# Optimization experiments

Hardware: AMD Instinct MI355X
Metric: run time of the kernel (lower is better)

Reference implementation:

```python
import jax, jax.numpy as jnp
import numpy as np

B, S, D = 4, 2048, 512
H = 8
DH = D // H
NEG = -9e15


def setup_inputs() -> dict:
    key = jax.random.key(0)
    ks = jax.random.split(key, 6)
    x = jax.random.normal(ks[0], (B, S, D), dtype=jnp.float32)
    mask = jax.random.randint(ks[1], (B, S), 0, 2, dtype=jnp.int32)
    # Linear params (torch convention: W [out, in], y = x @ W.T + b)
    lim_qkv = 1.0 / np.sqrt(D)
    W_qkv = jax.random.uniform(ks[2], (3 * D, D), jnp.float32, -lim_qkv, lim_qkv)
    b_qkv = jax.random.uniform(ks[3], (3 * D,), jnp.float32, -lim_qkv, lim_qkv)
    lim_o = 1.0 / np.sqrt(D)
    W_o = jax.random.uniform(ks[4], (D, D), jnp.float32, -lim_o, lim_o)
    b_o = jax.random.uniform(ks[5], (D,), jnp.float32, -lim_o, lim_o)
    return {"x": x, "mask": mask, "W_qkv": W_qkv, "b_qkv": b_qkv, "W_o": W_o, "b_o": b_o}


def reference(x, mask, W_qkv, b_qkv, W_o, b_o):
    b, s, d = x.shape
    # fused QKV projection: [B,S,3D]
    qkv = jnp.einsum('bsd,ed->bse', x, W_qkv) + b_qkv
    qkv = qkv.reshape(b, s, H, 3 * DH).transpose(0, 2, 1, 3)  # [B,H,S,3*DH]
    q, k, v = jnp.split(qkv, 3, axis=-1)  # each [B,H,S,DH]
    logits = jnp.einsum('bhqd,bhkd->bhqk', q, k) / jnp.sqrt(jnp.float32(DH))
    m = mask[:, None, None, :]  # [B,1,1,S]
    logits = jnp.where(m == 0, jnp.float32(NEG), logits)
    attn = jax.nn.softmax(logits, axis=-1)  # [B,H,S,S]
    values = jnp.einsum('bhqk,bhkd->bhqd', attn, v)
    values = values.transpose(0, 2, 1, 3).reshape(b, s, d)
    o = jnp.einsum('bsd,ed->bse', values, W_o) + b_o
    return o
```

## Files before the change

### kernel.cpp

```cpp
#include <hip/hip_runtime.h>
#include <stdint.h>

#define Bv 4
#define Sv 2048
#define Dv 512
#define Hv 8
#define E3 1536

typedef unsigned short u16;
typedef __bf16 bf16x8 __attribute__((ext_vector_type(8)));
typedef float f32x4 __attribute__((ext_vector_type(4)));

__device__ __forceinline__ u16 f2b(float f) {
  union { float f; uint32_t u; } v; v.f = f;
  uint32_t r = v.u + 0x7FFFu + ((v.u >> 16) & 1u);
  return (u16)(r >> 16);
}

__device__ __forceinline__ void gl_lds16(const void* g, void* l) {
  __builtin_amdgcn_global_load_lds(
      (__attribute__((address_space(1))) void*)(uintptr_t)g,
      (__attribute__((address_space(3))) void*)(uintptr_t)l, 16, 0, 0);
}

__global__ __launch_bounds__(256) void k_cast3(const float* __restrict__ x,
                                               const float* __restrict__ wqkv,
                                               const float* __restrict__ wo,
                                               const int* __restrict__ mask,
                                               u16* __restrict__ xb,
                                               u16* __restrict__ wqkvb,
                                               u16* __restrict__ wob,
                                               float* __restrict__ mbias) {
  const int bid = blockIdx.x;
  if (bid >= 2560) {
    const int i = (bid - 2560) * 256 + threadIdx.x;
    mbias[i] = mask[i] ? 0.0f : -1e30f;
    return;
  }
  const float* in; u16* out; int i;
  if (bid < 2048)      { in = x;    out = xb;    i = bid * 256 + threadIdx.x; }
  else if (bid < 2432) { in = wqkv; out = wqkvb; i = (bid - 2048) * 256 + threadIdx.x; }
  else                 { in = wo;   out = wob;   i = (bid - 2432) * 256 + threadIdx.x; }
  const float4* p = (const float4*)in;
  float4 a = p[(size_t)i * 2], b = p[(size_t)i * 2 + 1];
  union { u16 h[8]; uint4 v; } r;
  r.h[0] = f2b(a.x); r.h[1] = f2b(a.y); r.h[2] = f2b(a.z); r.h[3] = f2b(a.w);
  r.h[4] = f2b(b.x); r.h[5] = f2b(b.y); r.h[6] = f2b(b.z); r.h[7] = f2b(b.w);
  ((uint4*)out)[i] = r.v;
}

__global__ __launch_bounds__(256) void k_gemm_qkv(const u16* __restrict__ A,
                                                  const u16* __restrict__ Bw,
                                                  const float* __restrict__ bias,
                                                  u16* __restrict__ qp,
                                                  u16* __restrict__ kp,
                                                  u16* __restrict__ vp) {
  const int K = Dv, N = E3;
  __shared__ alignas(16) u16 As[128][32];
  __shared__ alignas(16) u16 Bs[128][32];
  const int tid = threadIdx.x, lane = tid & 63, w = tid >> 6;
  const int quad = lane >> 4, l16 = lane & 15;
  const int wm = w & 1, wn = w >> 1;
  const size_t m0 = (size_t)blockIdx.y * 128;
  const int n0 = blockIdx.x * 128;
  const int srow = lane >> 2, scol = (lane & 3) * 8;
  f32x4 acc[4][4] = {};
  for (int k0 = 0; k0 < K; k0 += 32) {
    #pragma unroll
    for (int c = 0; c < 2; ++c) {
      const int rb = (w * 2 + c) * 16;
      gl_lds16(A + (m0 + rb + srow) * K + k0 + scol, &As[rb][0]);
      gl_lds16(Bw + (size_t)(n0 + rb + srow) * K + k0 + scol, &Bs[rb][0]);
    }
    __syncthreads();
    bf16x8 af[4], bfr[4];
    #pragma unroll
    for (int t = 0; t < 4; ++t) {
      af[t]  = *(const bf16x8*)&As[wm * 64 + t * 16 + l16][quad * 8];
      bfr[t] = *(const bf16x8*)&Bs[wn * 64 + t * 16 + l16][quad * 8];
    }
    #pragma unroll
    for (int mt = 0; mt < 4; ++mt)
      #pragma unroll
      for (int nt = 0; nt < 4; ++nt)
        acc[mt][nt] = __builtin_amdgcn_mfma_f32_16x16x32_bf16(af[mt], bfr[nt],
                                                              acc[mt][nt], 0, 0, 0);
    __syncthreads();
  }
  #pragma unroll
  for (int nt = 0; nt < 4; ++nt) {
    const int cbase = n0 + wn * 64 + nt * 16;
    const int h = cbase / 192, rem = cbase % 192;
    const int region = rem >> 6;
    const int dh = (rem & 63) + l16;
    const float bv = bias[cbase + l16];
    #pragma unroll
    for (int mt = 0; mt < 4; ++mt) {
      #pragma unroll
      for (int r = 0; r < 4; ++r) {
        const int row = (int)m0 + wm * 64 + mt * 16 + quad * 4 + r;
        const u16 vb = f2b(acc[mt][nt][r] + bv);
        const int b = row >> 11, s = row & 2047;
        const size_t bhb = ((size_t)(b * 8 + h)) * 131072;
        if (region == 0) {
          qp[(size_t)row * 512 + h * 64 + dh] = vb;
        } else if (region == 1) {
          kp[bhb + (s >> 4) * 1024 + (dh >> 5) * 512 + ((dh >> 3) & 3) * 128 +
             (s & 15) * 8 + (dh & 7)] = vb;
        } else {
          vp[bhb + (s >> 5) * 2048 + (dh >> 4) * 512 + ((s >> 3) & 3) * 128 +
             (dh & 15) * 8 + (s & 7)] = vb;
        }
      }
    }
  }
}

__global__ __launch_bounds__(256) void k_gemm_out(const u16* __restrict__ A,
                                                  const u16* __restrict__ Bw,
                                                  const float* __restrict__ bias,
                                                  float* __restrict__ C) {
  const int K = Dv, N = Dv;
  __shared__ alignas(16) u16 As[64][32];
  __shared__ alignas(16) u16 Bs[128][32];
  const int tid = threadIdx.x, lane = tid & 63, w = tid >> 6;
  const int quad = lane >> 4, l16 = lane & 15;
  const size_t m0 = (size_t)blockIdx.y * 64;
  const int n0 = blockIdx.x * 128;
  const int srow = lane >> 2, scol = (lane & 3) * 8;
  f32x4 acc[4][2] = {};
  for (int k0 = 0; k0 < K; k0 += 32) {
    gl_lds16(A + (m0 + w * 16 + srow) * K + k0 + scol, &As[w * 16][0]);
    #pragma unroll
    for (int c = 0; c < 2; ++c) {
      const int rb = w * 32 + c * 16;
      gl_lds16(Bw + (size_t)(n0 + rb + srow) * K + k0 + scol, &Bs[rb][0]);
    }
    __syncthreads();
    bf16x8 af[4], bfr[2];
    #pragma unroll
    for (int t = 0; t < 4; ++t) af[t] = *(const bf16x8*)&As[t * 16 + l16][quad * 8];
    #pragma unroll
    for (int t = 0; t < 2; ++t)
      bfr[t] = *(const bf16x8*)&Bs[w * 32 + t * 16 + l16][quad * 8];
    #pragma unroll
    for (int mt = 0; mt < 4; ++mt)
      #pragma unroll
      for (int nt = 0; nt < 2; ++nt)
        acc[mt][nt] = __builtin_amdgcn_mfma_f32_16x16x32_bf16(af[mt], bfr[nt],
                                                              acc[mt][nt], 0, 0, 0);
    __syncthreads();
  }
  #pragma unroll
  for (int nt = 0; nt < 2; ++nt) {
    const int col = n0 + w * 32 + nt * 16 + l16;
    const float bv = bias[col];
    #pragma unroll
    for (int mt = 0; mt < 4; ++mt) {
      const size_t row = m0 + mt * 16 + quad * 4;
      #pragma unroll
      for (int r = 0; r < 4; ++r) C[(row + r) * N + col] = acc[mt][nt][r] + bv;
    }
  }
}

#define PPITCH 164
__global__ __launch_bounds__(256, 4) void k_attn(const u16* __restrict__ qp,
                                                 const u16* __restrict__ kp,
                                                 const u16* __restrict__ vp,
                                                 const float* __restrict__ mbias,
                                                 u16* __restrict__ vals) {
  __shared__ alignas(16) u16 Ps[4][16 * PPITCH];
  const int tid = threadIdx.x, lane = tid & 63, w = tid >> 6;
  const int quad = lane >> 4, l16 = lane & 15;
  const int bid = blockIdx.x;
  const int bh = bid & 31, strip = bid >> 5;
  const int b = bh >> 3, h = bh & 7;
  const int q0 = strip * 16;

  const u16* qrow = qp + (size_t)(b * Sv + q0 + l16) * 512 + h * 64 + quad * 8;
  bf16x8 aq0 = *(const bf16x8*)qrow;
  bf16x8 aq1 = *(const bf16x8*)(qrow + 32);

  bf16x8 bones;
  {
    union { u16 u; __bf16 b; } one; one.u = 0x3F80;
    #pragma unroll
    for (int j = 0; j < 8; ++j) bones[j] = one.b;
  }

  f32x4 La = {0.f, 0.f, 0.f, 0.f};
  f32x4 Oa[4] = {};

  const u16* kpb = kp + (size_t)bh * 131072 + lane * 8;
  const u16* vpb = vp + (size_t)bh * 131072 + lane * 8;
  const float* mrow = mbias + b * Sv + l16;
  u16* ps_w = &Ps[w][0];
  const float cs = 0.18033688011112042f;
  const int k_begin = w * (Sv / 4), k_end = k_begin + Sv / 4;

  #pragma unroll 1
  for (int k0 = k_begin; k0 < k_end; k0 += 128) {
    const int t0 = k0 >> 4, c0 = k0 >> 5;
    bf16x8 vv[2][4];
    #pragma unroll
    for (int ks = 0; ks < 2; ++ks)
      #pragma unroll
      for (int nt2 = 0; nt2 < 4; ++nt2)
        vv[ks][nt2] = *(const bf16x8*)(vpb + (size_t)((c0 + ks) * 4 + nt2) * 512);
    f32x4 Sa[8] = {};
    #pragma unroll
    for (int nt = 0; nt < 8; ++nt) {
      const u16* tb = kpb + (size_t)(t0 + nt) * 1024;
      bf16x8 bk0 = *(const bf16x8*)tb;
      bf16x8 bk1 = *(const bf16x8*)(tb + 512);
      Sa[nt] = __builtin_amdgcn_mfma_f32_16x16x32_bf16(aq0, bk0, Sa[nt], 0, 0, 0);
      Sa[nt] = __builtin_amdgcn_mfma_f32_16x16x32_bf16(aq1, bk1, Sa[nt], 0, 0, 0);
    }
    #pragma unroll
    for (int nt = 0; nt < 8; ++nt) {
      const float mb = mrow[k0 + nt * 16];
      #pragma unroll
      for (int r = 0; r < 4; ++r) {
        union { float f; uint32_t u; } pv;
        pv.f = __builtin_amdgcn_exp2f(fmaf(Sa[nt][r], cs, mb));
        ps_w[(quad * 4 + r) * PPITCH + nt * 16 + l16] = (u16)(pv.u >> 16);
      }
    }
    bf16x8 vv2[2][4];
    #pragma unroll
    for (int ks = 0; ks < 2; ++ks)
      #pragma unroll
      for (int nt2 = 0; nt2 < 4; ++nt2)
        vv2[ks][nt2] = *(const bf16x8*)(vpb + (size_t)((c0 + 2 + ks) * 4 + nt2) * 512);
    #pragma unroll
    for (int ks = 0; ks < 4; ++ks) {
      bf16x8 ap = *(const bf16x8*)(ps_w + l16 * PPITCH + ks * 32 + quad * 8);
      La = __builtin_amdgcn_mfma_f32_16x16x32_bf16(ap, bones, La, 0, 0, 0);
      #pragma unroll
      for (int nt2 = 0; nt2 < 4; ++nt2) {
        bf16x8 bv8 = (ks < 2) ? vv[ks][nt2] : vv2[ks - 2][nt2];
        Oa[nt2] = __builtin_amdgcn_mfma_f32_16x16x32_bf16(ap, bv8, Oa[nt2], 0, 0, 0);
      }
    }
  }

  if (w != 0) {
    f32x4* fl = (f32x4*)((float*)&Ps[w][0] + lane * 20);
    fl[0] = Oa[0]; fl[1] = Oa[1]; fl[2] = Oa[2]; fl[3] = Oa[3]; fl[4] = La;
  }
  __syncthreads();
  if (w == 0) {
    #pragma unroll
    for (int j = 1; j < 4; ++j) {
      const f32x4* fl = (const f32x4*)((const float*)&Ps[j][0] + lane * 20);
      #pragma unroll
      for (int i = 0; i < 4; ++i) Oa[i] += fl[i];
      La += fl[4];
    }
    float li[4];
    #pragma unroll
    for (int r = 0; r < 4; ++r) li[r] = 1.0f / La[r];
    #pragma unroll
    for (int nt2 = 0; nt2 < 4; ++nt2)
      #pragma unroll
      for (int r = 0; r < 4; ++r) {
        const size_t srow = (size_t)(b * Sv + q0 + quad * 4 + r);
        vals[srow * Dv + h * 64 + nt2 * 16 + l16] = f2b(Oa[nt2][r] * li[r]);
      }
  }
}

extern "C" void kernel_launch(void* const* d_in, const int* in_sizes, int n_in,
                              void* d_out, int out_size, void* d_ws, size_t ws_size,
                              hipStream_t stream) {
  const float* x    = (const float*)d_in[0];
  const int*   mask = (const int*)d_in[1];
  const float* Wqkv = (const float*)d_in[2];
  const float* bqkv = (const float*)d_in[3];
  const float* Wo   = (const float*)d_in[4];
  const float* bo   = (const float*)d_in[5];
  float* out = (float*)d_out;

  char* ws = (char*)d_ws;
  u16* xb    = (u16*)(ws + 0);
  u16* wqkvb = (u16*)(ws + 8388608);
  u16* wob   = (u16*)(ws + 9961472);
  u16* qp    = (u16*)(ws + 10485760);
  u16* kp    = (u16*)(ws + 18874368);
  u16* vp    = (u16*)(ws + 27262976);
  u16* vals  = (u16*)(ws + 35651584);
  float* mbias = (float*)(ws + 44040192);

  k_cast3<<<2592, 256, 0, stream>>>(x, Wqkv, Wo, mask, xb, wqkvb, wob, mbias);
  k_gemm_qkv<<<dim3(12, 64), 256, 0, stream>>>(xb, wqkvb, bqkv, qp, kp, vp);
  k_attn<<<4096, 256, 0, stream>>>(qp, kp, vp, mbias, vals);
  k_gemm_out<<<dim3(4, 128), 256, 0, stream>>>(vals, wob, bo, out);
}
```

Measured before the change: 204.1 us.

## Software-pipeline attention loop: overlap next QK^T MFMAs with current PV

```diff
diff --git a/kernel.cpp b/kernel.cpp
--- a/kernel.cpp
+++ b/kernel.cpp
@@ -55,7 +55,7 @@
                                                   u16* __restrict__ qp,
                                                   u16* __restrict__ kp,
                                                   u16* __restrict__ vp) {
-  const int K = Dv, N = E3;
+  const int K = Dv;
   __shared__ alignas(16) u16 As[128][32];
   __shared__ alignas(16) u16 Bs[128][32];
   const int tid = threadIdx.x, lane = tid & 63, w = tid >> 6;
@@ -165,7 +165,7 @@
 }
 
 #define PPITCH 164
-__global__ __launch_bounds__(256, 4) void k_attn(const u16* __restrict__ qp,
+__global__ __launch_bounds__(256, 3) void k_attn(const u16* __restrict__ qp,
                                                  const u16* __restrict__ kp,
                                                  const u16* __restrict__ vp,
                                                  const float* __restrict__ mbias,
@@ -191,35 +191,29 @@
 
   f32x4 La = {0.f, 0.f, 0.f, 0.f};
   f32x4 Oa[4] = {};
+  f32x4 Sa[8];
 
   const u16* kpb = kp + (size_t)bh * 131072 + lane * 8;
   const u16* vpb = vp + (size_t)bh * 131072 + lane * 8;
   const float* mrow = mbias + b * Sv + l16;
   u16* ps_w = &Ps[w][0];
   const float cs = 0.18033688011112042f;
-  const int k_begin = w * (Sv / 4), k_end = k_begin + Sv / 4;
-
-  #pragma unroll 1
-  for (int k0 = k_begin; k0 < k_end; k0 += 128) {
-    const int t0 = k0 >> 4, c0 = k0 >> 5;
-    bf16x8 vv[2][4];
-    #pragma unroll
-    for (int ks = 0; ks < 2; ++ks)
-      #pragma unroll
-      for (int nt2 = 0; nt2 < 4; ++nt2)
-        vv[ks][nt2] = *(const bf16x8*)(vpb + (size_t)((c0 + ks) * 4 + nt2) * 512);
-    f32x4 Sa[8] = {};
+  const int k_begin = w * (Sv / 4);
+
+  {
+    const int t0 = k_begin >> 4;
     #pragma unroll
     for (int nt = 0; nt < 8; ++nt) {
       const u16* tb = kpb + (size_t)(t0 + nt) * 1024;
       bf16x8 bk0 = *(const bf16x8*)tb;
       bf16x8 bk1 = *(const bf16x8*)(tb + 512);
-      Sa[nt] = __builtin_amdgcn_mfma_f32_16x16x32_bf16(aq0, bk0, Sa[nt], 0, 0, 0);
-      Sa[nt] = __builtin_amdgcn_mfma_f32_16x16x32_bf16(aq1, bk1, Sa[nt], 0, 0, 0);
+      f32x4 z = {0.f, 0.f, 0.f, 0.f};
+      z = __builtin_amdgcn_mfma_f32_16x16x32_bf16(aq0, bk0, z, 0, 0, 0);
+      Sa[nt] = __builtin_amdgcn_mfma_f32_16x16x32_bf16(aq1, bk1, z, 0, 0, 0);
     }
     #pragma unroll
     for (int nt = 0; nt < 8; ++nt) {
-      const float mb = mrow[k0 + nt * 16];
+      const float mb = mrow[k_begin + nt * 16];
       #pragma unroll
       for (int r = 0; r < 4; ++r) {
         union { float f; uint32_t u; } pv;
@@ -227,21 +221,70 @@
         ps_w[(quad * 4 + r) * PPITCH + nt * 16 + l16] = (u16)(pv.u >> 16);
       }
     }
-    bf16x8 vv2[2][4];
+  }
+
+  #pragma unroll 1
+  for (int i = 1; i < 4; ++i) {
+    const int k0 = k_begin + 128 * i;
+    const int t0 = k0 >> 4;
+    const int c0p = (k0 - 128) >> 5;
+    bf16x8 vv[4][4];
     #pragma unroll
     for (int ks = 0; ks < 2; ++ks)
       #pragma unroll
       for (int nt2 = 0; nt2 < 4; ++nt2)
-        vv2[ks][nt2] = *(const bf16x8*)(vpb + (size_t)((c0 + 2 + ks) * 4 + nt2) * 512);
+        vv[ks][nt2] = *(const bf16x8*)(vpb + (size_t)((c0p + ks) * 4 + nt2) * 512);
+    float mb[8];
+    #pragma unroll
+    for (int nt = 0; nt < 8; ++nt) mb[nt] = mrow[k0 + nt * 16];
+    #pragma unroll
+    for (int nt = 0; nt < 8; ++nt) {
+      const u16* tb = kpb + (size_t)(t0 + nt) * 1024;
+      bf16x8 bk0 = *(const bf16x8*)tb;
+      bf16x8 bk1 = *(const bf16x8*)(tb + 512);
+      f32x4 z = {0.f, 0.f, 0.f, 0.f};
+      z = __builtin_amdgcn_mfma_f32_16x16x32_bf16(aq0, bk0, z, 0, 0, 0);
+      Sa[nt] = __builtin_amdgcn_mfma_f32_16x16x32_bf16(aq1, bk1, z, 0, 0, 0);
+    }
+    #pragma unroll
+    for (int ks = 2; ks < 4; ++ks)
+      #pragma unroll
+      for (int nt2 = 0; nt2 < 4; ++nt2)
+        vv[ks][nt2] = *(const bf16x8*)(vpb + (size_t)((c0p + ks) * 4 + nt2) * 512);
     #pragma unroll
     for (int ks = 0; ks < 4; ++ks) {
       bf16x8 ap = *(const bf16x8*)(ps_w + l16 * PPITCH + ks * 32 + quad * 8);
       La = __builtin_amdgcn_mfma_f32_16x16x32_bf16(ap, bones, La, 0, 0, 0);
       #pragma unroll
-      for (int nt2 = 0; nt2 < 4; ++nt2) {
-        bf16x8 bv8 = (ks < 2) ? vv[ks][nt2] : vv2[ks - 2][nt2];
-        Oa[nt2] = __builtin_amdgcn_mfma_f32_16x16x32_bf16(ap, bv8, Oa[nt2], 0, 0, 0);
+      for (int nt2 = 0; nt2 < 4; ++nt2)
+        Oa[nt2] = __builtin_amdgcn_mfma_f32_16x16x32_bf16(ap, vv[ks][nt2], Oa[nt2], 0, 0, 0);
+    }
+    #pragma unroll
+    for (int nt = 0; nt < 8; ++nt) {
+      #pragma unroll
+      for (int r = 0; r < 4; ++r) {
+        union { float f; uint32_t u; } pv;
+        pv.f = __builtin_amdgcn_exp2f(fmaf(Sa[nt][r], cs, mb[nt]));
+        ps_w[(quad * 4 + r) * PPITCH + nt * 16 + l16] = (u16)(pv.u >> 16);
       }
+    }
+  }
+
+  {
+    const int c0p = (k_begin + 384) >> 5;
+    bf16x8 vv[4][4];
+    #pragma unroll
+    for (int ks = 0; ks < 4; ++ks)
+      #pragma unroll
+      for (int nt2 = 0; nt2 < 4; ++nt2)
+        vv[ks][nt2] = *(const bf16x8*)(vpb + (size_t)((c0p + ks) * 4 + nt2) * 512);
+    #pragma unroll
+    for (int ks = 0; ks < 4; ++ks) {
+      bf16x8 ap = *(const bf16x8*)(ps_w + l16 * PPITCH + ks * 32 + quad * 8);
+      La = __builtin_amdgcn_mfma_f32_16x16x32_bf16(ap, bones, La, 0, 0, 0);
+      #pragma unroll
+      for (int nt2 = 0; nt2 < 4; ++nt2)
+        Oa[nt2] = __builtin_amdgcn_mfma_f32_16x16x32_bf16(ap, vv[ks][nt2], Oa[nt2], 0, 0, 0);
     }
   }
 
```

Result: no change. 204.9 us (+0.4%).
